# Kernel optimization log

Hardware: AMD Instinct MI355X
Metric: run time of the kernel (lower is better)

The kernel has to match this reference:

```python
import jax, jax.numpy as jnp
import numpy as np

IMG = 768
SCORE_THR = 0.2
IOU_THR = 0.2
MAX_DET = 100  # fixed-size keep buffer (jit-compatible stand-in for dynamic keep list)


def make_anchors(img=IMG, strides=(8, 16, 32, 64, 128), anchor_scale=4.0):
    """EfficientDet anchors, y1x1y2x2 (matches Anchors module semantics)."""
    scales = (2.0 ** 0, 2.0 ** (1.0 / 3.0), 2.0 ** (2.0 / 3.0))
    ratios = ((1.0, 1.0), (1.4, 0.7), (0.7, 1.4))
    out = []
    for stride in strides:
        for s in scales:
            for rx, ry in ratios:
                base = anchor_scale * stride * s
                ax, ay = base * rx / 2.0, base * ry / 2.0
                xv = np.arange(stride / 2.0, img, stride)
                xx, yy = np.meshgrid(xv, xv)
                out.append(np.stack([yy - ay, xx - ax, yy + ay, xx + ax], -1).reshape(-1, 4))
    return np.concatenate(out, 0).astype(np.float32)  # [A,4]


def setup_inputs() -> dict:
    key = jax.random.key(0)
    k1, k2, k3 = jax.random.split(key, 3)
    A, C = 110484, 80
    x = jax.random.normal(k1, (1, 3, IMG, IMG), jnp.float32)
    regression = jax.random.normal(k2, (1, A, 4), jnp.float32) * 0.1
    classification = jax.random.normal(k3, (1, A, C), jnp.float32) - 5.0
    anchors = jnp.asarray(make_anchors())[None]  # [1,A,4]
    return {"x": x, "regression": regression, "classification": classification, "anchors": anchors}


def _decode_clip(x, regression, anchors):
    ya = (anchors[..., 0] + anchors[..., 2]) * 0.5
    xa = (anchors[..., 1] + anchors[..., 3]) * 0.5
    ha = anchors[..., 2] - anchors[..., 0]
    wa = anchors[..., 3] - anchors[..., 1]
    w = jnp.exp(regression[..., 3]) * wa
    h = jnp.exp(regression[..., 2]) * ha
    yc = regression[..., 0] * ha + ya
    xc = regression[..., 1] * wa + xa
    H, W = x.shape[2], x.shape[3]
    # ClipBoxes: x1,y1 >= 0 ; x2 <= W ; y2 <= H. Output x1y1x2y2.
    x1 = jnp.clip(xc - w * 0.5, 0.0, None)
    y1 = jnp.clip(yc - h * 0.5, 0.0, None)
    x2 = jnp.clip(xc + w * 0.5, None, float(W))
    y2 = jnp.clip(yc + h * 0.5, None, float(H))
    return jnp.stack([x1, y1, x2, y2], axis=-1)


def _nms(boxes, scores):
    """Greedy NMS. boxes [A,4] x1y1x2y2, scores [A] (-1 for below-threshold).
    Returns (keep_idx [MAX_DET] into original anchor order, keep_valid [MAX_DET])."""
    order = jnp.argsort(-scores)
    b = boxes[order]
    s = scores[order]
    area = (b[:, 2] - b[:, 0]) * (b[:, 3] - b[:, 1])
    keep_idx = jnp.zeros((MAX_DET,), jnp.int32)
    keep_valid = jnp.zeros((MAX_DET,), bool)
    active = s > 0.0

    def body(i, carry):
        active, keep_idx, keep_valid = carry
        sa = jnp.where(active, s, -1.0)
        j = jnp.argmax(sa)            # highest remaining score
        ok = sa[j] > 0.0              # any candidate left?
        keep_idx = keep_idx.at[i].set(jnp.where(ok, order[j].astype(jnp.int32), 0))
        keep_valid = keep_valid.at[i].set(ok)
        cb = b[j]
        ix1 = jnp.maximum(cb[0], b[:, 0])
        iy1 = jnp.maximum(cb[1], b[:, 1])
        ix2 = jnp.minimum(cb[2], b[:, 2])
        iy2 = jnp.minimum(cb[3], b[:, 3])
        inter = jnp.clip(ix2 - ix1, 0.0, None) * jnp.clip(iy2 - iy1, 0.0, None)
        iou = inter / (area[j] + area - inter + 1e-8)
        # torch keeps only ious < IOU_THR; current box (iou=1) is also removed
        active = active & (iou < IOU_THR) & ok
        return active, keep_idx, keep_valid

    _, keep_idx, keep_valid = jax.lax.fori_loop(0, MAX_DET, body, (active, keep_idx, keep_valid))
    return keep_idx, keep_valid


def reference(x, regression, classification, anchors):
    cls = jax.nn.sigmoid(classification)          # [1,A,C]
    boxes = _decode_clip(x, regression, anchors)  # [1,A,4]
    s = jnp.max(cls[0], axis=1)                   # per-anchor max class score
    s = jnp.where(s > SCORE_THR, s, -1.0)         # score threshold (mask instead of gather)
    keep_idx, keep_valid = _nms(boxes[0], s)
    kc = cls[0][keep_idx]                         # [MAX_DET, C]
    kscores = jnp.max(kc, axis=1)
    klabels = jnp.argmax(kc, axis=1)
    kboxes = boxes[0][keep_idx]
    v = keep_valid
    boxes_out = jnp.where(v[:, None], kboxes, 0.0)[None]   # [1,MAX_DET,4]
    scores_out = jnp.where(v, kscores, 0.0)[None]          # [1,MAX_DET]
    labels_out = jnp.where(v, klabels, 0)[None]            # [1,MAX_DET] int
    return boxes_out, scores_out, labels_out
```

## Files before the change

### kernel.cpp

```cpp
#include <hip/hip_runtime.h>
#include <hip/hip_bf16.h>

#define A_TOTAL 110484
#define NCLS 80
#define CAP 2048
#define NW 26
#define SWEEP_CAP (NW * 64)
#define MAX_DETS 100
#define IMGF 768.0f
#define IOU_T 0.2f

struct Ws {
    int count;
    int pad[3];
    unsigned long long key[CAP];
    float4 box[CAP];
    int label[CAP];
    unsigned long long skey[CAP];
    float4 sbox[CAP];
    int slabel[CAP];
    unsigned long long M[SWEEP_CAP * NW];
};

__global__ void score_decode_kernel(const float* __restrict__ cls,
                                    const float* __restrict__ reg,
                                    const float* __restrict__ anc,
                                    Ws* __restrict__ ws) {
    int gid = blockIdx.x * blockDim.x + threadIdx.x;
    int a = gid >> 2;
    int sub = gid & 3;
    if (a >= A_TOTAL) return;

    const float4* row = (const float4*)(cls + (size_t)a * NCLS);
    float m = -1e30f;
    int lbl = 0;
#pragma unroll
    for (int q = 0; q < 5; ++q) {
        float4 v = row[sub + q * 4];
        int c0 = (sub + q * 4) * 4;
        if (v.x > m) { m = v.x; lbl = c0 + 0; }
        if (v.y > m) { m = v.y; lbl = c0 + 1; }
        if (v.z > m) { m = v.z; lbl = c0 + 2; }
        if (v.w > m) { m = v.w; lbl = c0 + 3; }
    }

    unsigned int mb = __float_as_uint(m);
    mb ^= (mb & 0x80000000u) ? 0xFFFFFFFFu : 0x80000000u;
    unsigned long long key =
        ((unsigned long long)mb << 32) | (unsigned int)(0xFFFFFFFFu - (unsigned int)lbl);
#pragma unroll
    for (int d = 1; d < 4; d <<= 1) {
        unsigned long long o = __shfl_xor(key, d, 64);
        if (o > key) key = o;
    }
    if (sub != 0) return;

    unsigned int hb = (unsigned int)(key >> 32);
    hb ^= (hb & 0x80000000u) ? 0x80000000u : 0xFFFFFFFFu;
    m = __uint_as_float(hb);
    lbl = (int)(0xFFFFFFFFu - (unsigned int)(key & 0xFFFFFFFFu));

    float sig = 1.0f / (1.0f + expf(-m));
    if (!(sig > 0.2f)) return;

    float4 ab = ((const float4*)anc)[a];
    float4 rb = ((const float4*)reg)[a];
    float ya = __fmul_rn(__fadd_rn(ab.x, ab.z), 0.5f);
    float xa = __fmul_rn(__fadd_rn(ab.y, ab.w), 0.5f);
    float ha = __fsub_rn(ab.z, ab.x);
    float wa = __fsub_rn(ab.w, ab.y);
    float w = __fmul_rn(expf(rb.w), wa);
    float h = __fmul_rn(expf(rb.z), ha);
    float yc = __fadd_rn(__fmul_rn(rb.x, ha), ya);
    float xc = __fadd_rn(__fmul_rn(rb.y, wa), xa);
    float x1 = fmaxf(__fsub_rn(xc, __fmul_rn(w, 0.5f)), 0.0f);
    float y1 = fmaxf(__fsub_rn(yc, __fmul_rn(h, 0.5f)), 0.0f);
    float x2 = fminf(__fadd_rn(xc, __fmul_rn(w, 0.5f)), IMGF);
    float y2 = fminf(__fadd_rn(yc, __fmul_rn(h, 0.5f)), IMGF);

    int pos = atomicAdd(&ws->count, 1);
    if (pos < CAP) {
        ws->key[pos] = ((unsigned long long)__float_as_uint(sig) << 32) |
                       (unsigned int)(0xFFFFFFFFu - (unsigned int)a);
        ws->box[pos] = make_float4(x1, y1, x2, y2);
        ws->label[pos] = lbl;
    }
}

__global__ __launch_bounds__(256) void rank_kernel(Ws* __restrict__ ws) {
    __shared__ unsigned long long kl[CAP];
    int tid = threadIdx.x;
    int n = ws->count;
    if (n > CAP) n = CAP;

    for (int j = tid; j < n; j += 256) kl[j] = ws->key[j];
    __syncthreads();

    int i = blockIdx.x * 256 + tid;
    if (i >= n) return;

    unsigned long long my = kl[i];
    int r = 0;
    int j = 0;
    for (; j + 8 <= n; j += 8) {
        r += (kl[j + 0] > my) ? 1 : 0;
        r += (kl[j + 1] > my) ? 1 : 0;
        r += (kl[j + 2] > my) ? 1 : 0;
        r += (kl[j + 3] > my) ? 1 : 0;
        r += (kl[j + 4] > my) ? 1 : 0;
        r += (kl[j + 5] > my) ? 1 : 0;
        r += (kl[j + 6] > my) ? 1 : 0;
        r += (kl[j + 7] > my) ? 1 : 0;
    }
    for (; j < n; ++j) r += (kl[j] > my) ? 1 : 0;

    ws->skey[r] = my;
    ws->sbox[r] = ws->box[i];
    ws->slabel[r] = ws->label[i];
}

__global__ __launch_bounds__(256) void mask_kernel(Ws* __restrict__ ws) {
    int gw = (blockIdx.x * 256 + threadIdx.x) >> 6;
    int lane = threadIdx.x & 63;
    if (gw >= SWEEP_CAP * NW) return;
    int i = gw / NW;
    int w = gw - i * NW;
    int n = ws->count;
    if (n > CAP) n = CAP;
    if (n > SWEEP_CAP) n = SWEEP_CAP;
    if (i >= n) {
        if (lane == 0) ws->M[gw] = 0ull;
        return;
    }

    float4 kb = ws->sbox[i];
    float ka = __fmul_rn(__fsub_rn(kb.z, kb.x), __fsub_rn(kb.w, kb.y));
    int j = (w << 6) | lane;
    float4 cb = ws->sbox[j];
    float ca = __fmul_rn(__fsub_rn(cb.z, cb.x), __fsub_rn(cb.w, cb.y));
    float ix1 = fmaxf(kb.x, cb.x);
    float iy1 = fmaxf(kb.y, cb.y);
    float ix2 = fminf(kb.z, cb.z);
    float iy2 = fminf(kb.w, cb.w);
    float iw = fmaxf(__fsub_rn(ix2, ix1), 0.0f);
    float ih = fmaxf(__fsub_rn(iy2, iy1), 0.0f);
    float inter = __fmul_rn(iw, ih);
    float denom = __fadd_rn(__fadd_rn(__fadd_rn(ka, ca), -inter), 1e-8f);
    float iou = __fdiv_rn(inter, denom);
    unsigned long long bal = __ballot(!(iou < IOU_T));
    if (lane == 0) ws->M[gw] = bal;
}

__global__ __launch_bounds__(64, 1) void sweep_kernel(const Ws* __restrict__ ws,
                                                      float* __restrict__ out) {
    int lane = threadIdx.x;
    int n = ws->count;
    if (n > CAP) n = CAP;
    if (n > SWEEP_CAP) n = SWEEP_CAP;

    unsigned long long act;
    {
        int rem = n - (lane << 6);
        act = (rem >= 64) ? ~0ull : ((rem > 0) ? ((1ull << rem) - 1ull) : 0ull);
        if (lane >= NW) act = 0ull;
    }

    int k0 = 0, k1 = 0, nk = 0;

    for (int w = 0; w < NW && nk < MAX_DETS; ++w) {
        unsigned int lo = __builtin_amdgcn_readlane((unsigned int)(act & 0xFFFFFFFFull), w);
        unsigned int hi = __builtin_amdgcn_readlane((unsigned int)(act >> 32), w);
        unsigned long long aw = ((unsigned long long)hi << 32) | lo;
        while (aw) {
            int b = __builtin_ctzll(aw);
            int i = (w << 6) | b;
            if (nk < 64) { if (lane == nk) k0 = i; }
            else         { if (lane == nk - 64) k1 = i; }
            ++nk;
            if (nk >= MAX_DETS) break;
            unsigned long long rowm = (lane < NW) ? ws->M[(size_t)i * NW + lane] : 0ull;
            act &= ~rowm;
            lo = __builtin_amdgcn_readlane((unsigned int)(act & 0xFFFFFFFFull), w);
            hi = __builtin_amdgcn_readlane((unsigned int)(act >> 32), w);
            aw = (((unsigned long long)hi << 32) | lo) & ~((2ull << b) - 1ull);
        }
    }

    for (int o = lane; o < MAX_DETS; o += 64) {
        float b0 = 0.f, b1 = 0.f, b2 = 0.f, b3 = 0.f, sc = 0.f, lb = 0.f;
        int pick = (o < 64) ? k0 : k1;
        if (o < nk) {
            float4 bb = ws->sbox[pick];
            b0 = bb.x; b1 = bb.y; b2 = bb.z; b3 = bb.w;
            sc = __uint_as_float((unsigned int)(ws->skey[pick] >> 32));
            lb = (float)ws->slabel[pick];
        }
        out[o * 4 + 0] = b0;
        out[o * 4 + 1] = b1;
        out[o * 4 + 2] = b2;
        out[o * 4 + 3] = b3;
        out[400 + o] = sc;
        out[500 + o] = lb;
    }
}

extern "C" void kernel_launch(void* const* d_in, const int* in_sizes, int n_in,
                              void* d_out, int out_size, void* d_ws, size_t ws_size,
                              hipStream_t stream) {
    const float* reg = (const float*)d_in[1];
    const float* cls = (const float*)d_in[2];
    const float* anc = (const float*)d_in[3];
    Ws* ws = (Ws*)d_ws;

    hipMemsetAsync(d_ws, 0, sizeof(int), stream);

    int blocks = (A_TOTAL * 4 + 255) / 256;
    score_decode_kernel<<<blocks, 256, 0, stream>>>(cls, reg, anc, ws);
    rank_kernel<<<CAP / 256, 256, 0, stream>>>(ws);
    mask_kernel<<<(SWEEP_CAP * NW + 3) / 4, 256, 0, stream>>>(ws);
    sweep_kernel<<<1, 64, 0, stream>>>(ws, (float*)d_out);
}
```

Before: 159.7 us.

## Batch greedy NMS sweep over eight candidates with speculative mask row loads

The single-wave sweep now gathers up to eight still-active candidates at a time and issues their eight suppression-mask row loads together. It then commits them in order, skipping any candidate already suppressed by an earlier commit in the same batch. The goal is to hide the serial global-memory latency of one row load per kept box. The cost is extra speculative loads and more register pressure and control flow.

```diff
diff --git a/kernel.cpp b/kernel.cpp
--- a/kernel.cpp
+++ b/kernel.cpp
@@ -166,23 +166,81 @@
     }
 
     int k0 = 0, k1 = 0, nk = 0;
-
-    for (int w = 0; w < NW && nk < MAX_DETS; ++w) {
-        unsigned int lo = __builtin_amdgcn_readlane((unsigned int)(act & 0xFFFFFFFFull), w);
-        unsigned int hi = __builtin_amdgcn_readlane((unsigned int)(act >> 32), w);
-        unsigned long long aw = ((unsigned long long)hi << 32) | lo;
-        while (aw) {
-            int b = __builtin_ctzll(aw);
-            int i = (w << 6) | b;
-            if (nk < 64) { if (lane == nk) k0 = i; }
-            else         { if (lane == nk - 64) k1 = i; }
-            ++nk;
-            if (nk >= MAX_DETS) break;
-            unsigned long long rowm = (lane < NW) ? ws->M[(size_t)i * NW + lane] : 0ull;
-            act &= ~rowm;
-            lo = __builtin_amdgcn_readlane((unsigned int)(act & 0xFFFFFFFFull), w);
-            hi = __builtin_amdgcn_readlane((unsigned int)(act >> 32), w);
-            aw = (((unsigned long long)hi << 32) | lo) & ~((2ull << b) - 1ull);
+    int pos = -1;
+
+    while (nk < MAX_DETS) {
+        int c0 = 0, c1 = 0, c2 = 0, c3 = 0, c4 = 0, c5 = 0, c6 = 0, c7 = 0;
+        int ncand = 0;
+        int w0 = (pos + 1) >> 6;
+        for (int w = w0; w < NW && ncand < 8; ++w) {
+            unsigned int lo = __builtin_amdgcn_readlane((unsigned int)(act & 0xFFFFFFFFull), w);
+            unsigned int hi = __builtin_amdgcn_readlane((unsigned int)(act >> 32), w);
+            unsigned long long aw = ((unsigned long long)hi << 32) | lo;
+            if (pos >= 0 && w == (pos >> 6)) aw &= ~((2ull << (pos & 63)) - 1ull);
+            while (aw && ncand < 8) {
+                int b = __builtin_ctzll(aw);
+                aw &= aw - 1ull;
+                int idx = (w << 6) | b;
+                switch (ncand) {
+                    case 0: c0 = idx; break;
+                    case 1: c1 = idx; break;
+                    case 2: c2 = idx; break;
+                    case 3: c3 = idx; break;
+                    case 4: c4 = idx; break;
+                    case 5: c5 = idx; break;
+                    case 6: c6 = idx; break;
+                    default: c7 = idx; break;
+                }
+                ++ncand;
+            }
+        }
+        if (ncand == 0) break;
+
+        unsigned long long r0 = 0, r1 = 0, r2 = 0, r3 = 0, r4 = 0, r5 = 0, r6 = 0, r7 = 0;
+        if (lane < NW) {
+            r0 = ws->M[(size_t)c0 * NW + lane];
+            r1 = ws->M[(size_t)c1 * NW + lane];
+            r2 = ws->M[(size_t)c2 * NW + lane];
+            r3 = ws->M[(size_t)c3 * NW + lane];
+            r4 = ws->M[(size_t)c4 * NW + lane];
+            r5 = ws->M[(size_t)c5 * NW + lane];
+            r6 = ws->M[(size_t)c6 * NW + lane];
+            r7 = ws->M[(size_t)c7 * NW + lane];
+        }
+
+        unsigned long long sup = 0ull;
+#define COMMIT(S, CS, RS)                                                                 \
+        if (S < ncand && nk < MAX_DETS) {                                                 \
+            unsigned int slo = __builtin_amdgcn_readlane((unsigned int)(sup & 0xFFFFFFFFull), (CS) >> 6); \
+            unsigned int shi = __builtin_amdgcn_readlane((unsigned int)(sup >> 32), (CS) >> 6);           \
+            unsigned long long sw = ((unsigned long long)shi << 32) | slo;                \
+            if (!((sw >> ((CS) & 63)) & 1ull)) {                                          \
+                if (nk < 64) { if (lane == nk) k0 = (CS); }                               \
+                else         { if (lane == nk - 64) k1 = (CS); }                          \
+                ++nk;                                                                     \
+                sup |= (RS);                                                              \
+            }                                                                             \
+        }
+        COMMIT(0, c0, r0)
+        COMMIT(1, c1, r1)
+        COMMIT(2, c2, r2)
+        COMMIT(3, c3, r3)
+        COMMIT(4, c4, r4)
+        COMMIT(5, c5, r5)
+        COMMIT(6, c6, r6)
+        COMMIT(7, c7, r7)
+#undef COMMIT
+        act &= ~sup;
+
+        switch (ncand) {
+            case 1: pos = c0; break;
+            case 2: pos = c1; break;
+            case 3: pos = c2; break;
+            case 4: pos = c3; break;
+            case 5: pos = c4; break;
+            case 6: pos = c5; break;
+            case 7: pos = c6; break;
+            default: pos = c7; break;
         }
     }
 
```

Result: faster. 153.1 us (-4.2%).
